# Kernel optimization log

Measured on AMD Instinct MI355X. Metric: run time of the kernel, lower is better.

The kernel has to match this reference:

```python
import jax, jax.numpy as jnp
import numpy as np

B, XD, ZD, XE, H, NH = 8192, 4096, 1024, 64, 128, 4
NUM_STEPS, STEP, NOISE = 10, 0.01, 1.0
EPS = 1e-5


def setup_inputs() -> dict:
    key = jax.random.key(0)
    ks = jax.random.split(key, 16)
    w = lambda k, s: jax.random.normal(k, s, jnp.float32) * 0.02
    inp = {"x": jax.random.normal(ks[0], (B, XD), jnp.float32)}
    inp.update(
        px_W1=w(ks[1], (H, ZD)), px_b1=jnp.zeros(H, jnp.float32),
        px_W2=w(ks[2], (XD, H)), px_b2=jnp.zeros(XD, jnp.float32),
        emb_W=w(ks[3], (XE, XD)), emb_b=jnp.zeros(XE, jnp.float32),
        xp_W=w(ks[4], (H, XE)), xp_b=jnp.zeros(H, jnp.float32),
        zp_W=w(ks[5], (H, ZD)), zp_b=jnp.zeros(H, jnp.float32),
        sa_Wqkv=w(ks[6], (3 * H, H)), sa_bqkv=jnp.zeros(3 * H, jnp.float32),
        sa_Wo=w(ks[7], (H, H)), sa_bo=jnp.zeros(H, jnp.float32),
        ca_Wqkv=w(ks[8], (3 * H, H)), ca_bqkv=jnp.zeros(3 * H, jnp.float32),
        ca_Wo=w(ks[9], (H, H)), ca_bo=jnp.zeros(H, jnp.float32),
        ffn_W1=w(ks[10], (H, H)), ffn_b1=jnp.zeros(H, jnp.float32),
        ffn_W2=w(ks[11], (H, H)), ffn_b2=jnp.zeros(H, jnp.float32),
        ln1_g=jnp.ones(H, jnp.float32), ln1_b=jnp.zeros(H, jnp.float32),
        ln2_g=jnp.ones(H, jnp.float32), ln2_b=jnp.zeros(H, jnp.float32),
        ln3_g=jnp.ones(H, jnp.float32), ln3_b=jnp.zeros(H, jnp.float32),
        out_W=w(ks[12], (1, H)), out_b=jnp.zeros(1, jnp.float32),
    )
    return inp


def _ln(x, g, b):
    m = jnp.mean(x, -1, keepdims=True)
    v = jnp.var(x, -1, keepdims=True)
    return (x - m) * jax.lax.rsqrt(v + EPS) * g + b


def _mha(q, k, v, Wqkv, bqkv, Wo, bo):
    # torch nn.MultiheadAttention math, batch-first layout (B, S, E)
    E = q.shape[-1]
    d = E // NH
    Wq, Wk, Wv = jnp.split(Wqkv, 3, 0)
    bq, bk, bv = jnp.split(bqkv, 3, 0)
    hd = lambda t, W, bb: (t @ W.T + bb).reshape(t.shape[0], t.shape[1], NH, d)
    qh, kh, vh = hd(q, Wq, bq), hd(k, Wk, bk), hd(v, Wv, bv)
    s = jnp.einsum('bqhd,bkhd->bhqk', qh, kh) / jnp.sqrt(jnp.float32(d))
    a = jax.nn.softmax(s, -1)
    o = jnp.einsum('bhqk,bkhd->bqhd', a, vh).reshape(q.shape[0], q.shape[1], E)
    return o @ Wo.T + bo


def _forward(x, px_W1, px_b1, px_W2, px_b2, emb_W, emb_b, xp_W, xp_b, zp_W, zp_b,
             sa_Wqkv, sa_bqkv, sa_Wo, sa_bo, ca_Wqkv, ca_bqkv, ca_Wo, ca_bo,
             ffn_W1, ffn_b1, ffn_W2, ffn_b2, ln1_g, ln1_b, ln2_g, ln2_b,
             ln3_g, ln3_b, out_W, out_b):
    bsz = x.shape[0]
    px = lambda z: jax.nn.relu(z @ px_W1.T + px_b1) @ px_W2.T + px_b2
    grad_fn = jax.grad(lambda z: jnp.sum((px(z) - x) ** 2))
    ks = jax.random.split(jax.random.key(42), NUM_STEPS + 1)
    z0 = jax.random.normal(ks[0], (bsz, ZD), jnp.float32)

    def step(z, k):
        z = z - 0.5 * STEP * grad_fn(z)
        z = z + NOISE * jnp.sqrt(jnp.float32(STEP)) * jax.random.normal(k, z.shape, z.dtype)
        return z, None

    z, _ = jax.lax.scan(step, z0, ks[1:])
    z = jax.lax.stop_gradient(z)  # torch: z.detach()

    x_recon = px(z)                               # (B, XD)
    x_tok = (x @ emb_W.T + emb_b)[:, None, :]     # (B, 1, XE)
    z_lat = z[:, None, :]                         # (B, 1, ZD)
    x_h = x_tok @ xp_W.T + xp_b                   # (B, 1, H)
    z_h = z_lat @ zp_W.T + zp_b                   # (B, 1, H)
    sa = _mha(x_h, x_h, x_h, sa_Wqkv, sa_bqkv, sa_Wo, sa_bo)
    h1 = _ln(x_h + sa, ln1_g, ln1_b)
    ca = _mha(h1, z_h, z_h, ca_Wqkv, ca_bqkv, ca_Wo, ca_bo)
    h2 = _ln(h1 + ca, ln2_g, ln2_b)
    ff = jax.nn.relu(h2 @ ffn_W1.T + ffn_b1) @ ffn_W2.T + ffn_b2
    h3 = _ln(h2 + ff, ln3_g, ln3_b)
    y_pred = h3 @ out_W.T + out_b                 # (B, 1, 1)
    return x_recon, y_pred


def reference(x, px_W1, px_b1, px_W2, px_b2, emb_W, emb_b, xp_W, xp_b, zp_W, zp_b,
              sa_Wqkv, sa_bqkv, sa_Wo, sa_bo, ca_Wqkv, ca_bqkv, ca_Wo, ca_bo,
              ffn_W1, ffn_b1, ffn_W2, ffn_b2, ln1_g, ln1_b, ln2_g, ln2_b,
              ln3_g, ln3_b, out_W, out_b):
    return _forward(x, px_W1, px_b1, px_W2, px_b2, emb_W, emb_b, xp_W, xp_b,
                    zp_W, zp_b, sa_Wqkv, sa_bqkv, sa_Wo, sa_bo, ca_Wqkv,
                    ca_bqkv, ca_Wo, ca_bo, ffn_W1, ffn_b1, ffn_W2, ffn_b2,
                    ln1_g, ln1_b, ln2_g, ln2_b, ln3_g, ln3_b, out_W, out_b)
```

## Files before the change

### kernel.cpp

```cpp
#include <hip/hip_runtime.h>
#include <hip/hip_bf16.h>
#include <cstdint>
#include <cstddef>
#include <cmath>

#define B_     8192
#define XD_    4096
#define ZD_    1024
#define XE_    64
#define H_     128
#define ZN_    (B_*ZD_)

typedef __attribute__((ext_vector_type(8))) short short8_t;
typedef __attribute__((ext_vector_type(4))) float f32x4_t;
#define MFMA16(a,b,c) __builtin_amdgcn_mfma_f32_16x16x32_bf16((a),(b),(c),0,0,0)

__host__ __device__ __forceinline__ uint32_t rotl32_(uint32_t x, int r){ return (x<<r)|(x>>(32-r)); }

__host__ __device__ __forceinline__ void tf2x32(uint32_t k0, uint32_t k1,
                                                uint32_t x0, uint32_t x1,
                                                uint32_t* o0, uint32_t* o1){
  uint32_t k2 = k0 ^ k1 ^ 0x1BD11BDAu;
  x0 += k0; x1 += k1;
  x0 += x1; x1 = rotl32_(x1,13); x1 ^= x0;
  x0 += x1; x1 = rotl32_(x1,15); x1 ^= x0;
  x0 += x1; x1 = rotl32_(x1,26); x1 ^= x0;
  x0 += x1; x1 = rotl32_(x1, 6); x1 ^= x0;
  x0 += k1; x1 += k2 + 1u;
  x0 += x1; x1 = rotl32_(x1,17); x1 ^= x0;
  x0 += x1; x1 = rotl32_(x1,29); x1 ^= x0;
  x0 += x1; x1 = rotl32_(x1,16); x1 ^= x0;
  x0 += x1; x1 = rotl32_(x1,24); x1 ^= x0;
  x0 += k2; x1 += k0 + 2u;
  x0 += x1; x1 = rotl32_(x1,13); x1 ^= x0;
  x0 += x1; x1 = rotl32_(x1,15); x1 ^= x0;
  x0 += x1; x1 = rotl32_(x1,26); x1 ^= x0;
  x0 += x1; x1 = rotl32_(x1, 6); x1 ^= x0;
  x0 += k0; x1 += k1 + 3u;
  x0 += x1; x1 = rotl32_(x1,17); x1 ^= x0;
  x0 += x1; x1 = rotl32_(x1,29); x1 ^= x0;
  x0 += x1; x1 = rotl32_(x1,16); x1 ^= x0;
  x0 += x1; x1 = rotl32_(x1,24); x1 ^= x0;
  x0 += k1; x1 += k2 + 4u;
  x0 += x1; x1 = rotl32_(x1,13); x1 ^= x0;
  x0 += x1; x1 = rotl32_(x1,15); x1 ^= x0;
  x0 += x1; x1 = rotl32_(x1,26); x1 ^= x0;
  x0 += x1; x1 = rotl32_(x1, 6); x1 ^= x0;
  x0 += k2; x1 += k0 + 5u;
  *o0 = x0; *o1 = x1;
}

__device__ __forceinline__ float erfinv_(float x){
  float w = -__logf(fmaf(-x, x, 1.0f));
  float p;
  if (w < 5.0f){
    w -= 2.5f;
    p = 2.81022636e-08f;
    p = fmaf(p, w, 3.43273939e-07f);
    p = fmaf(p, w, -3.5233877e-06f);
    p = fmaf(p, w, -4.39150654e-06f);
    p = fmaf(p, w, 0.00021858087f);
    p = fmaf(p, w, -0.00125372503f);
    p = fmaf(p, w, -0.00417768164f);
    p = fmaf(p, w, 0.246640727f);
    p = fmaf(p, w, 1.50140941f);
  } else {
    w = sqrtf(w) - 3.0f;
    p = -0.000200214257f;
    p = fmaf(p, w, 0.000100950558f);
    p = fmaf(p, w, 0.00134934322f);
    p = fmaf(p, w, -0.00367342844f);
    p = fmaf(p, w, 0.00573950773f);
    p = fmaf(p, w, -0.0076224613f);
    p = fmaf(p, w, 0.00943887047f);
    p = fmaf(p, w, 1.00167406f);
    p = fmaf(p, w, 2.83297682f);
  }
  return p * x;
}

__device__ __forceinline__ float bits_to_normal(uint32_t bits){
  float f = __uint_as_float((bits >> 9) | 0x3f800000u) - 1.0f;
  float u = fmaxf(-0.99999994f, fmaf(f, 2.0f, -0.99999994f));
  return 1.41421356f * erfinv_(u);
}

__device__ __forceinline__ float rng_normal(uint32_t k0, uint32_t k1, uint32_t idx){
  uint32_t o0, o1; tf2x32(k0, k1, 0u, idx, &o0, &o1);
  return bits_to_normal(o0 ^ o1);
}

__device__ __forceinline__ ushort f2bf(float f){
  return __builtin_bit_cast(ushort, __float2bfloat16(f));
}

__global__ void k_prepA(const float* __restrict__ saWo, const float* __restrict__ saWqkv,
                        const float* __restrict__ caWo, const float* __restrict__ caWqkv,
                        float* __restrict__ S, float* __restrict__ U){
  int blk = blockIdx.x, tid = threadIdx.x;
  int idx = (blk & 255) * 64 + tid;
  int i = idx >> 7, j = idx & 127;
  if (blk < 256){
    float acc = (i == j) ? 1.0f : 0.0f;
    for (int k = 0; k < H_; ++k) acc += saWo[i*H_ + k] * saWqkv[(2*H_ + k)*H_ + j];
    S[idx] = acc;
  } else {
    float acc = 0.0f;
    for (int k = 0; k < H_; ++k) acc += caWo[i*H_ + k] * caWqkv[(2*H_ + k)*H_ + j];
    U[idx] = acc;
  }
}

__global__ void k_prepB(const float* __restrict__ saWo, const float* __restrict__ sabqkv, const float* __restrict__ sabo,
                        const float* __restrict__ caWo, const float* __restrict__ cabqkv, const float* __restrict__ cabo,
                        const float* __restrict__ W2, const float* __restrict__ pb2,
                        float* __restrict__ s0, float* __restrict__ u0, float* __restrict__ cb,
                        uint32_t* __restrict__ dkeys){
  int blk = blockIdx.x, tid = threadIdx.x;
  if (blk == 0 && tid == 0){
    for (uint32_t i = 0; i < 11; ++i){
      uint32_t a, b; tf2x32(0u, 42u, 0u, i, &a, &b);
      dkeys[2*i] = a; dkeys[2*i+1] = b;
    }
  }
  if (blk < 2){
    int i = blk*64 + tid;
    float acc = sabo[i];
    for (int k = 0; k < H_; ++k) acc += saWo[i*H_ + k] * sabqkv[2*H_ + k];
    s0[i] = acc;
  } else if (blk < 4){
    int i = (blk-2)*64 + tid;
    float acc = cabo[i];
    for (int k = 0; k < H_; ++k) acc += caWo[i*H_ + k] * cabqkv[2*H_ + k];
    u0[i] = acc;
  } else {
    int j = (blk-4)*64 + tid;
    float acc = 0.0f;
    for (int c = 0; c < XD_; ++c) acc += pb2[c] * W2[(size_t)c*H_ + j];
    cb[j] = acc;
  }
}

__global__ void k_prepM(const float* __restrict__ W2, float* __restrict__ M){
  int idx = blockIdx.x*64 + threadIdx.x;
  int j1 = idx >> 7, j2 = idx & 127;
  float acc = 0.0f;
  for (int c = 0; c < XD_; ++c) acc += W2[(size_t)c*H_ + j1] * W2[(size_t)c*H_ + j2];
  M[idx] = acc;
}

__global__ void k_prepTR(const float* __restrict__ S, const float* __restrict__ U,
                         const float* __restrict__ xpW, const float* __restrict__ zpW,
                         const float* __restrict__ xpb, const float* __restrict__ zpb,
                         const float* __restrict__ s0, const float* __restrict__ u0,
                         float* __restrict__ T, float* __restrict__ R,
                         float* __restrict__ t0, float* __restrict__ r0v){
  int blk = blockIdx.x, tid = threadIdx.x;
  if (blk < 128){
    int idx = blk*64 + tid;
    int i = idx >> 6, e = idx & 63;
    float acc = 0.0f;
    for (int m = 0; m < H_; ++m) acc += S[i*H_ + m] * xpW[m*XE_ + e];
    T[idx] = acc;
  } else if (blk < 2176){
    int idx = (blk-128)*64 + tid;
    int i = idx >> 10, k = idx & 1023;
    float acc = 0.0f;
    for (int m = 0; m < H_; ++m) acc += U[i*H_ + m] * zpW[(size_t)m*ZD_ + k];
    R[idx] = acc;
  } else if (blk < 2178){
    int i = (blk-2176)*64 + tid;
    float acc = s0[i];
    for (int m = 0; m < H_; ++m) acc += S[i*H_ + m] * xpb[m];
    t0[i] = acc;
  } else {
    int i = (blk-2178)*64 + tid;
    float acc = u0[i];
    for (int m = 0; m < H_; ++m) acc += U[i*H_ + m] * zpb[m];
    r0v[i] = acc;
  }
}

__global__ void k_prepWXT(const float* __restrict__ W2, const float* __restrict__ T,
                          const float* __restrict__ embW, const float* __restrict__ embb,
                          const float* __restrict__ t0,
                          ushort* __restrict__ WXT, float* __restrict__ q0){
  int idx = blockIdx.x*256 + threadIdx.x;
  int j = idx >> 12, c = idx & 4095;
  float v;
  if (j < H_) v = W2[(size_t)c*H_ + j];
  else {
    int i = j - H_;
    float acc = 0.0f;
    for (int e = 0; e < XE_; ++e) acc += T[i*XE_ + e] * embW[(size_t)e*XD_ + c];
    v = acc;
  }
  WXT[idx] = f2bf(v);
  if (idx < H_){
    float acc = t0[idx];
    for (int e = 0; e < XE_; ++e) acc += T[idx*XE_ + e] * embb[e];
    q0[idx] = acc;
  }
}

__global__ void k_conv(const float* __restrict__ W2, const float* __restrict__ W1,
                       const float* __restrict__ Mm, const float* __restrict__ R,
                       ushort* __restrict__ W2bf, ushort* __restrict__ W1bf,
                       ushort* __restrict__ W1Tbf, ushort* __restrict__ Mbf,
                       ushort* __restrict__ FBT){
  int idx = blockIdx.x*256 + threadIdx.x;
  if (idx < 524288) W2bf[idx] = f2bf(W2[idx]);
  else if (idx < 655360){ int i = idx - 524288; W1bf[i] = f2bf(W1[i]); }
  else if (idx < 786432){ int i = idx - 655360; int k = i >> 7, h = i & 127;
    W1Tbf[i] = f2bf(W1[h*ZD_ + k]); }
  else if (idx < 802816){ int i = idx - 786432; Mbf[i] = f2bf(Mm[i]); }
  else { int i = idx - 802816; int j = i >> 10, k = i & 1023;
    FBT[i] = f2bf(j < H_ ? W1[j*ZD_ + k] : R[(size_t)(j-H_)*ZD_ + k]); }
}

__global__ __launch_bounds__(256) void k_xpass_mfma(
    const float* __restrict__ x, const ushort* __restrict__ WXT,
    const float* __restrict__ cb, const float* __restrict__ q0,
    float* __restrict__ cneg, float* __restrict__ h1pre){
  __shared__ __align__(16) ushort xt[2][32*72];
  __shared__ __align__(16) ushort bt[2][128*72];
  const int t = threadIdx.x, lane = t & 63, w = t >> 6;
  const int bm = blockIdx.x >> 1, bn = blockIdx.x & 1;
  const int row0 = bm*32, ncol0 = bn*128;
  const int l15 = lane & 15, kq8 = (lane >> 4)*8, rq = (lane >> 4)*4;
  const int rt = w & 1, cb4 = (w >> 1)*4;
  const int xr = t >> 3, xk = (t & 7)*8;
  const int wn = t >> 1, wk = (t & 1)*32;
  f32x4_t acc[4] = {};
  {
    float4 v0 = *(const float4*)&x[(size_t)(row0+xr)*XD_ + xk];
    float4 v1 = *(const float4*)&x[(size_t)(row0+xr)*XD_ + xk + 4];
    union { ushort u[8]; uint4 q; } p;
    p.u[0]=f2bf(v0.x); p.u[1]=f2bf(v0.y); p.u[2]=f2bf(v0.z); p.u[3]=f2bf(v0.w);
    p.u[4]=f2bf(v1.x); p.u[5]=f2bf(v1.y); p.u[6]=f2bf(v1.z); p.u[7]=f2bf(v1.w);
    *(uint4*)&xt[0][xr*72 + xk] = p.q;
    const ushort* s = &WXT[(size_t)(ncol0+wn)*XD_ + wk];
    uint4 b0v=*(const uint4*)s, b1v=*(const uint4*)(s+8), b2v=*(const uint4*)(s+16), b3v=*(const uint4*)(s+24);
    ushort* d = &bt[0][wn*72 + wk];
    *(uint4*)d=b0v; *(uint4*)(d+8)=b1v; *(uint4*)(d+16)=b2v; *(uint4*)(d+24)=b3v;
  }
  float4 xv0, xv1; uint4 wb0, wb1, wb2, wb3;
  {
    xv0 = *(const float4*)&x[(size_t)(row0+xr)*XD_ + 64 + xk];
    xv1 = *(const float4*)&x[(size_t)(row0+xr)*XD_ + 64 + xk + 4];
    const ushort* s = &WXT[(size_t)(ncol0+wn)*XD_ + 64 + wk];
    wb0=*(const uint4*)s; wb1=*(const uint4*)(s+8); wb2=*(const uint4*)(s+16); wb3=*(const uint4*)(s+24);
  }
  #pragma unroll 1
  for (int it = 0; it < 64; ++it){
    __syncthreads();
    if (it < 63){
      union { ushort u[8]; uint4 q; } p;
      p.u[0]=f2bf(xv0.x); p.u[1]=f2bf(xv0.y); p.u[2]=f2bf(xv0.z); p.u[3]=f2bf(xv0.w);
      p.u[4]=f2bf(xv1.x); p.u[5]=f2bf(xv1.y); p.u[6]=f2bf(xv1.z); p.u[7]=f2bf(xv1.w);
      *(uint4*)&xt[(it+1)&1][xr*72 + xk] = p.q;
      ushort* d = &bt[(it+1)&1][wn*72 + wk];
      *(uint4*)d=wb0; *(uint4*)(d+8)=wb1; *(uint4*)(d+16)=wb2; *(uint4*)(d+24)=wb3;
    }
    if (it < 62){
      const int kt = (it+2)*64;
      xv0 = *(const float4*)&x[(size_t)(row0+xr)*XD_ + kt + xk];
      xv1 = *(const float4*)&x[(size_t)(row0+xr)*XD_ + kt + xk + 4];
      const ushort* s = &WXT[(size_t)(ncol0+wn)*XD_ + kt + wk];
      wb0=*(const uint4*)s; wb1=*(const uint4*)(s+8); wb2=*(const uint4*)(s+16); wb3=*(const uint4*)(s+24);
    }
    const ushort* xb = &xt[it&1][(rt*16+l15)*72];
    const ushort* bb = &bt[it&1][0];
    #pragma unroll
    for (int h = 0; h < 2; ++h){
      short8_t a = *(const short8_t*)(xb + h*32 + kq8);
      #pragma unroll
      for (int c = 0; c < 4; ++c){
        short8_t b = *(const short8_t*)(bb + ((cb4+c)*16+l15)*72 + h*32 + kq8);
        acc[c] = MFMA16(a, b, acc[c]);
      }
    }
  }
  #pragma unroll
  for (int c = 0; c < 4; ++c){
    int jl = (cb4+c)*16 + l15;
    #pragma unroll
    for (int r = 0; r < 4; ++r){
      int row = row0 + rt*16 + rq + r;
      float v = acc[c][r];
      if (bn == 0) cneg[(size_t)row*H_ + jl] = 2.0f*(cb[jl] - v);
      else         h1pre[(size_t)row*H_ + jl] = v + q0[jl];
    }
  }
}

__global__ __launch_bounds__(512) void k_langevin(
    const ushort* __restrict__ W1bf, const ushort* __restrict__ W1Tbf,
    const ushort* __restrict__ Mbf, const ushort* __restrict__ FBT,
    const float* __restrict__ b1, const float* __restrict__ r0v,
    const float* __restrict__ cneg, const uint32_t* __restrict__ dkeys,
    ushort* __restrict__ hfin_bf, float* __restrict__ capre){
  __shared__ __align__(16) float  zlds[16][1028];
  __shared__ __align__(16) ushort zbf[16][1032];
  __shared__ __align__(16) ushort ws_[2][128*72];
  __shared__ __align__(16) ushort abuf[16*136];
  __shared__ __align__(16) ushort glbuf[16*136];

  const int t = threadIdx.x, lane = t & 63, w = t >> 6;
  const int l15 = lane & 15, kq8 = (lane >> 4)*8, rq = (lane >> 4)*4;
  const int b0 = blockIdx.x * 16;
  const int myc = w*16 + l15;

  {
    const uint32_t k0 = dkeys[0], k1 = dkeys[1];
    const int row16 = t >> 5, c4 = (t & 31)*4;
    #pragma unroll 1
    for (int i = 0; i < 8; ++i){
      const int col = c4 + 128*i;
      uint32_t base = (uint32_t)(b0 + row16)*1024u + (uint32_t)col;
      float4 v;
      v.x = rng_normal(k0,k1,base+0);
      v.y = rng_normal(k0,k1,base+1);
      v.z = rng_normal(k0,k1,base+2);
      v.w = rng_normal(k0,k1,base+3);
      *(float4*)&zlds[row16][col] = v;
      ushort4 b4; b4.x=f2bf(v.x); b4.y=f2bf(v.y); b4.z=f2bf(v.z); b4.w=f2bf(v.w);
      *(ushort4*)&zbf[row16][col] = b4;
    }
  }
  const float bb = b1[myc];
  float cn[4];
  #pragma unroll
  for (int r = 0; r < 4; ++r) cn[r] = cneg[(size_t)(b0+rq+r)*H_ + myc];

  const int wr = t >> 2, wk4 = (t & 3)*16;
  const int kk3 = (t & 3)*32;

  #pragma unroll 1
  for (int s = 0; s < 10; ++s){
    const uint32_t nk0 = dkeys[2+2*s], nk1 = dkeys[3+2*s];
    {
      const ushort* sw = &W1bf[(size_t)wr*ZD_ + wk4];
      uint4 a0 = *(const uint4*)sw, a1 = *(const uint4*)(sw+8);
      ushort* d = &ws_[0][wr*72 + wk4];
      *(uint4*)d = a0; *(uint4*)(d+8) = a1;
    }
    uint4 p0, p1;
    {
      const ushort* sw = &W1bf[(size_t)wr*ZD_ + 64 + wk4];
      p0 = *(const uint4*)sw; p1 = *(const uint4*)(sw+8);
    }
    f32x4_t acc = {};
    #pragma unroll 1
    for (int it = 0; it < 16; ++it){
      __syncthreads();
      if (it < 15){
        ushort* d = &ws_[(it+1)&1][wr*72 + wk4];
        *(uint4*)d = p0; *(uint4*)(d+8) = p1;
      }
      if (it < 14){
        const ushort* sw = &W1bf[(size_t)wr*ZD_ + (it+2)*64 + wk4];
        p0 = *(const uint4*)sw; p1 = *(const uint4*)(sw+8);
      }
      const ushort* wsb = &ws_[it&1][myc*72];
      #pragma unroll
      for (int h = 0; h < 2; ++h){
        short8_t av = *(const short8_t*)&zbf[l15][it*64 + h*32 + kq8];
        short8_t bv = *(const short8_t*)(wsb + h*32 + kq8);
        acc = MFMA16(av, bv, acc);
      }
    }
    float hv[4];
    #pragma unroll
    for (int r = 0; r < 4; ++r){
      hv[r] = acc[r] + bb;
      abuf[(rq+r)*136 + myc] = f2bf(hv[r] > 0.f ? hv[r] : 0.f);
    }
    __syncthreads();
    {
      const ushort* sm = &Mbf[(size_t)wr*H_ + kk3];
      uint4 m0=*(const uint4*)sm, m1=*(const uint4*)(sm+8), m2=*(const uint4*)(sm+16), m3=*(const uint4*)(sm+24);
      ushort* d = &ws_[kk3>>6][wr*72 + (kk3&63)];
      *(uint4*)d=m0; *(uint4*)(d+8)=m1; *(uint4*)(d+16)=m2; *(uint4*)(d+24)=m3;
    }
    __syncthreads();
    f32x4_t acc2 = {};
    #pragma unroll
    for (int c = 0; c < 2; ++c)
      #pragma unroll
      for (int h = 0; h < 2; ++h){
        short8_t av = *(const short8_t*)&abuf[l15*136 + c*64 + h*32 + kq8];
        short8_t bv = *(const short8_t*)&ws_[c][myc*72 + h*32 + kq8];
        acc2 = MFMA16(av, bv, acc2);
      }
    #pragma unroll
    for (int r = 0; r < 4; ++r){
      float g = (hv[r] > 0.f) ? fmaf(2.f, acc2[r], cn[r]) : 0.f;
      glbuf[(rq+r)*136 + myc] = f2bf(g);
    }
    uint4 v0, v1, v2, v3;
    {
      const ushort* sw = &W1Tbf[(size_t)wr*H_ + kk3];
      v0=*(const uint4*)sw; v1=*(const uint4*)(sw+8); v2=*(const uint4*)(sw+16); v3=*(const uint4*)(sw+24);
    }
    #pragma unroll 1
    for (int nt = 0; nt < 8; ++nt){
      __syncthreads();
      {
        ushort* d = &ws_[kk3>>6][wr*72 + (kk3&63)];
        *(uint4*)d=v0; *(uint4*)(d+8)=v1; *(uint4*)(d+16)=v2; *(uint4*)(d+24)=v3;
      }
      if (nt < 7){
        const ushort* sw = &W1Tbf[(size_t)((nt+1)*128 + wr)*H_ + kk3];
        v0=*(const uint4*)sw; v1=*(const uint4*)(sw+8); v2=*(const uint4*)(sw+16); v3=*(const uint4*)(sw+24);
      }
      __syncthreads();
      f32x4_t acc3 = {};
      #pragma unroll
      for (int c = 0; c < 2; ++c)
        #pragma unroll
        for (int h = 0; h < 2; ++h){
          short8_t av = *(const short8_t*)&glbuf[l15*136 + c*64 + h*32 + kq8];
          short8_t bv = *(const short8_t*)&ws_[c][myc*72 + h*32 + kq8];
          acc3 = MFMA16(av, bv, acc3);
        }
      const int col = nt*128 + myc;
      #pragma unroll
      for (int r = 0; r < 4; ++r){
        const int row = rq + r;
        uint32_t idx = (uint32_t)(b0+row)*1024u + (uint32_t)col;
        float t2 = fmaf(-0.005f, acc3[r], zlds[row][col]);
        float zn = fmaf(0.1f, rng_normal(nk0,nk1,idx), t2);
        zlds[row][col] = zn;
        zbf[row][col] = f2bf(zn);
      }
    }
    __syncthreads();
  }

  f32x4_t fac0 = {}, fac1 = {};
  const int n2 = t >> 1, kh = (t & 1)*32;
  uint4 c0, c1, c2, c3;
  {
    const ushort* sf = &FBT[(size_t)n2*ZD_ + kh];
    c0=*(const uint4*)sf; c1=*(const uint4*)(sf+8); c2=*(const uint4*)(sf+16); c3=*(const uint4*)(sf+24);
  }
  #pragma unroll 1
  for (int it = 0; it < 16; ++it){
    __syncthreads();
    {
      ushort* d = (n2 < 128) ? &ws_[0][n2*72 + kh] : &ws_[1][(n2-128)*72 + kh];
      *(uint4*)d=c0; *(uint4*)(d+8)=c1; *(uint4*)(d+16)=c2; *(uint4*)(d+24)=c3;
    }
    if (it < 15){
      const ushort* sf = &FBT[(size_t)n2*ZD_ + (it+1)*64 + kh];
      c0=*(const uint4*)sf; c1=*(const uint4*)(sf+8); c2=*(const uint4*)(sf+16); c3=*(const uint4*)(sf+24);
    }
    __syncthreads();
    #pragma unroll
    for (int h = 0; h < 2; ++h){
      short8_t av = *(const short8_t*)&zbf[l15][it*64 + h*32 + kq8];
      short8_t bv0 = *(const short8_t*)&ws_[0][myc*72 + h*32 + kq8];
      fac0 = MFMA16(av, bv0, fac0);
      short8_t bv1 = *(const short8_t*)&ws_[1][myc*72 + h*32 + kq8];
      fac1 = MFMA16(av, bv1, fac1);
    }
  }
  {
    const float rv = r0v[myc];
    #pragma unroll
    for (int r = 0; r < 4; ++r){
      int row = b0 + rq + r;
      float h0 = fac0[r] + bb;
      hfin_bf[(size_t)row*H_ + myc] = f2bf(h0 > 0.f ? h0 : 0.f);
      capre[(size_t)row*H_ + myc] = fac1[r] + rv;
    }
  }
}

__global__ __launch_bounds__(256) void k_xrecon_mfma(
    const ushort* __restrict__ hfin_bf, const ushort* __restrict__ W2bf,
    const float* __restrict__ b2, float* __restrict__ out){
  __shared__ __align__(16) ushort at[64*136];
  __shared__ __align__(16) ushort bt[128*136];
  const int tid = threadIdx.x, lane = tid & 63, w = tid >> 6;
  const int bm = blockIdx.x >> 5, bn = blockIdx.x & 31;
  const int row0 = bm*64, c0 = bn*128;
  const int l15 = lane & 15, kq8 = (lane >> 4)*8, rq = (lane >> 4)*4;
  { int r = tid >> 2, kq = (tid & 3)*32;
    const ushort* src = &hfin_bf[(size_t)(row0 + r)*H_ + kq];
    #pragma unroll
    for (int i = 0; i < 4; ++i) *(uint4*)&at[r*136 + kq + 8*i] = *(const uint4*)(src + 8*i);
  }
  { int n = tid >> 1, kh = (tid & 1)*64;
    const ushort* src = &W2bf[(size_t)(c0 + n)*H_ + kh];
    #pragma unroll
    for (int i = 0; i < 8; ++i) *(uint4*)&bt[n*136 + kh + 8*i] = *(const uint4*)(src + 8*i);
  }
  __syncthreads();
  f32x4_t acc[8] = {};
  #pragma unroll
  for (int k = 0; k < 4; ++k){
    short8_t a = *(const short8_t*)&at[(w*16 + l15)*136 + k*32 + kq8];
    #pragma unroll
    for (int nf = 0; nf < 8; ++nf){
      short8_t b = *(const short8_t*)&bt[(nf*16 + l15)*136 + k*32 + kq8];
      acc[nf] = MFMA16(a, b, acc[nf]);
    }
  }
  #pragma unroll
  for (int nf = 0; nf < 8; ++nf){
    int c = c0 + nf*16 + l15;
    float bbv = b2[c];
    #pragma unroll
    for (int r = 0; r < 4; ++r){
      int row = row0 + w*16 + rq + r;
      out[(size_t)row*XD_ + c] = acc[nf][r] + bbv;
    }
  }
}

__device__ __forceinline__ float wsum64(float v){
  #pragma unroll
  for (int off = 32; off > 0; off >>= 1) v += __shfl_xor(v, off, 64);
  return v;
}

__global__ __launch_bounds__(256) void k_tail(
    const float* __restrict__ h1pre, const float* __restrict__ capre,
    const float* __restrict__ ln1g, const float* __restrict__ ln1b,
    const float* __restrict__ ln2g, const float* __restrict__ ln2b,
    const float* __restrict__ ln3g, const float* __restrict__ ln3b,
    const float* __restrict__ fW1, const float* __restrict__ fb1,
    const float* __restrict__ fW2, const float* __restrict__ fb2,
    const float* __restrict__ outW, const float* __restrict__ outb,
    float* __restrict__ y){
  __shared__ float sh2[4][128];
  __shared__ float st1[4][128];
  const int tid = threadIdx.x;
  const int w = tid >> 6;
  const int l = tid & 63;
  const int b = blockIdx.x * 4 + w;
  const float* hp = h1pre + (size_t)b * H_;
  const float* cp = capre + (size_t)b * H_;
  float x0 = hp[l], x1 = hp[l+64];
  float m = wsum64(x0 + x1) * (1.0f/128.0f);
  float d0 = x0 - m, d1 = x1 - m;
  float v = wsum64(d0*d0 + d1*d1) * (1.0f/128.0f);
  float rs = rsqrtf(v + 1e-5f);
  float h1a = d0 * rs * ln1g[l]    + ln1b[l];
  float h1b = d1 * rs * ln1g[l+64] + ln1b[l+64];
  x0 = h1a + cp[l]; x1 = h1b + cp[l+64];
  m = wsum64(x0 + x1) * (1.0f/128.0f);
  d0 = x0 - m; d1 = x1 - m;
  v = wsum64(d0*d0 + d1*d1) * (1.0f/128.0f);
  rs = rsqrtf(v + 1e-5f);
  float h2a = d0 * rs * ln2g[l]    + ln2b[l];
  float h2b = d1 * rs * ln2g[l+64] + ln2b[l+64];
  sh2[w][l] = h2a; sh2[w][l+64] = h2b;
  __syncthreads();
  float ta = fb1[l], tb = fb1[l+64];
  #pragma unroll 8
  for (int m4 = 0; m4 < H_; m4 += 4){
    float4 hv = *(const float4*)&sh2[w][m4];
    float4 wa = *(const float4*)&fW1[(size_t)l*H_ + m4];
    float4 wb = *(const float4*)&fW1[(size_t)(l+64)*H_ + m4];
    ta = fmaf(wa.x, hv.x, ta); ta = fmaf(wa.y, hv.y, ta); ta = fmaf(wa.z, hv.z, ta); ta = fmaf(wa.w, hv.w, ta);
    tb = fmaf(wb.x, hv.x, tb); tb = fmaf(wb.y, hv.y, tb); tb = fmaf(wb.z, hv.z, tb); tb = fmaf(wb.w, hv.w, tb);
  }
  ta = fmaxf(ta, 0.0f); tb = fmaxf(tb, 0.0f);
  st1[w][l] = ta; st1[w][l+64] = tb;
  __syncthreads();
  float fa = fb2[l], fbv = fb2[l+64];
  #pragma unroll 8
  for (int m4 = 0; m4 < H_; m4 += 4){
    float4 tv = *(const float4*)&st1[w][m4];
    float4 wa = *(const float4*)&fW2[(size_t)l*H_ + m4];
    float4 wb = *(const float4*)&fW2[(size_t)(l+64)*H_ + m4];
    fa  = fmaf(wa.x, tv.x, fa);  fa  = fmaf(wa.y, tv.y, fa);  fa  = fmaf(wa.z, tv.z, fa);  fa  = fmaf(wa.w, tv.w, fa);
    fbv = fmaf(wb.x, tv.x, fbv); fbv = fmaf(wb.y, tv.y, fbv); fbv = fmaf(wb.z, tv.z, fbv); fbv = fmaf(wb.w, tv.w, fbv);
  }
  x0 = h2a + fa; x1 = h2b + fbv;
  m = wsum64(x0 + x1) * (1.0f/128.0f);
  d0 = x0 - m; d1 = x1 - m;
  v = wsum64(d0*d0 + d1*d1) * (1.0f/128.0f);
  rs = rsqrtf(v + 1e-5f);
  float h3a = d0 * rs * ln3g[l]    + ln3b[l];
  float h3b = d1 * rs * ln3g[l+64] + ln3b[l+64];
  float py = wsum64(outW[l]*h3a + outW[l+64]*h3b);
  if (l == 0) y[b] = py + outb[0];
}

extern "C" void kernel_launch(void* const* d_in, const int* in_sizes, int n_in,
                              void* d_out, int out_size, void* d_ws, size_t ws_size,
                              hipStream_t stream){
  const float* x      = (const float*)d_in[0];
  const float* pxW1   = (const float*)d_in[1];
  const float* pxb1   = (const float*)d_in[2];
  const float* pxW2   = (const float*)d_in[3];
  const float* pxb2   = (const float*)d_in[4];
  const float* embW   = (const float*)d_in[5];
  const float* embb   = (const float*)d_in[6];
  const float* xpW    = (const float*)d_in[7];
  const float* xpb    = (const float*)d_in[8];
  const float* zpW    = (const float*)d_in[9];
  const float* zpb    = (const float*)d_in[10];
  const float* saWqkv = (const float*)d_in[11];
  const float* sabqkv = (const float*)d_in[12];
  const float* saWo   = (const float*)d_in[13];
  const float* sabo   = (const float*)d_in[14];
  const float* caWqkv = (const float*)d_in[15];
  const float* cabqkv = (const float*)d_in[16];
  const float* caWo   = (const float*)d_in[17];
  const float* cabo   = (const float*)d_in[18];
  const float* fW1    = (const float*)d_in[19];
  const float* fb1    = (const float*)d_in[20];
  const float* fW2    = (const float*)d_in[21];
  const float* fb2    = (const float*)d_in[22];
  const float* ln1g   = (const float*)d_in[23];
  const float* ln1b   = (const float*)d_in[24];
  const float* ln2g   = (const float*)d_in[25];
  const float* ln2b   = (const float*)d_in[26];
  const float* ln3g   = (const float*)d_in[27];
  const float* ln3b   = (const float*)d_in[28];
  const float* outW   = (const float*)d_in[29];
  const float* outb   = (const float*)d_in[30];
  (void)in_sizes; (void)n_in; (void)out_size; (void)ws_size;

  float* ws    = (float*)d_ws;
  float* cneg  = ws;
  float* h1pre = cneg + (size_t)B_*H_;
  float* capre = h1pre + (size_t)B_*H_;
  float* Rm    = capre + (size_t)B_*H_;
  float* Mm    = Rm + (size_t)H_*ZD_;
  float* Sm    = Mm + H_*H_;
  float* Um    = Sm + H_*H_;
  float* Tm    = Um + H_*H_;
  float* vs0   = Tm + H_*XE_;
  float* vu0   = vs0 + H_;
  float* vt0   = vu0 + H_;
  float* vq0   = vt0 + H_;
  float* vr0   = vq0 + H_;
  float* vcb   = vr0 + H_;
  uint32_t* dkeys = (uint32_t*)(vcb + H_);
  ushort* WXT   = (ushort*)(dkeys + 32);
  ushort* W2bf  = WXT + (size_t)256*XD_;
  ushort* W1bf  = W2bf + (size_t)XD_*H_;
  ushort* W1Tbf = W1bf + (size_t)H_*ZD_;
  ushort* Mbf   = W1Tbf + (size_t)ZD_*H_;
  ushort* FBT   = Mbf + H_*H_;
  ushort* hfin  = FBT + (size_t)256*ZD_;

  float* xre   = (float*)d_out;
  float* ypred = xre + (size_t)B_*XD_;

  k_prepA   <<<512,  64, 0, stream>>>(saWo, saWqkv, caWo, caWqkv, Sm, Um);
  k_prepB   <<<6,    64, 0, stream>>>(saWo, sabqkv, sabo, caWo, cabqkv, cabo, pxW2, pxb2,
                                      vs0, vu0, vcb, dkeys);
  k_prepM   <<<256,  64, 0, stream>>>(pxW2, Mm);
  k_prepTR  <<<2180, 64, 0, stream>>>(Sm, Um, xpW, zpW, xpb, zpb, vs0, vu0, Tm, Rm, vt0, vr0);
  k_prepWXT <<<4096, 256, 0, stream>>>(pxW2, Tm, embW, embb, vt0, WXT, vq0);
  k_conv    <<<4160, 256, 0, stream>>>(pxW2, pxW1, Mm, Rm, W2bf, W1bf, W1Tbf, Mbf, FBT);
  k_xpass_mfma <<<512, 256, 0, stream>>>(x, WXT, vcb, vq0, cneg, h1pre);
  k_langevin <<<512, 512, 0, stream>>>(W1bf, W1Tbf, Mbf, FBT, pxb1, vr0, cneg, dkeys, hfin, capre);
  k_xrecon_mfma <<<4096, 256, 0, stream>>>(hfin, W2bf, pxb2, xre);
  k_tail    <<<2048, 256, 0, stream>>>(h1pre, capre, ln1g, ln1b, ln2g, ln2b, ln3g, ln3b,
                                       fW1, fb1, fW2, fb2, outW, outb, ypred);
}
```

Before: 919.8 us.

## Run Langevin dynamics in projected 256-dim space using precomputed Gram matrices

```diff
diff --git a/kernel.cpp b/kernel.cpp
--- a/kernel.cpp
+++ b/kernel.cpp
@@ -93,6 +93,7 @@
 __device__ __forceinline__ ushort f2bf(float f){
   return __builtin_bit_cast(ushort, __float2bfloat16(f));
 }
+__device__ __forceinline__ float bf2f(ushort u){ return __uint_as_float(((uint32_t)u) << 16); }
 
 __global__ void k_prepA(const float* __restrict__ saWo, const float* __restrict__ saWqkv,
                         const float* __restrict__ caWo, const float* __restrict__ caWqkv,
@@ -205,17 +206,26 @@
 
 __global__ void k_conv(const float* __restrict__ W2, const float* __restrict__ W1,
                        const float* __restrict__ Mm, const float* __restrict__ R,
-                       ushort* __restrict__ W2bf, ushort* __restrict__ W1bf,
-                       ushort* __restrict__ W1Tbf, ushort* __restrict__ Mbf,
+                       ushort* __restrict__ W2bf, ushort* __restrict__ Mbf,
                        ushort* __restrict__ FBT){
   int idx = blockIdx.x*256 + threadIdx.x;
   if (idx < 524288) W2bf[idx] = f2bf(W2[idx]);
-  else if (idx < 655360){ int i = idx - 524288; W1bf[i] = f2bf(W1[i]); }
-  else if (idx < 786432){ int i = idx - 655360; int k = i >> 7, h = i & 127;
-    W1Tbf[i] = f2bf(W1[h*ZD_ + k]); }
-  else if (idx < 802816){ int i = idx - 786432; Mbf[i] = f2bf(Mm[i]); }
-  else { int i = idx - 802816; int j = i >> 10, k = i & 1023;
+  else if (idx < 540672){ int i = idx - 524288; Mbf[i] = f2bf(2.0f*Mm[i]); }
+  else { int i = idx - 540672; int j = i >> 10, k = i & 1023;
     FBT[i] = f2bf(j < H_ ? W1[j*ZD_ + k] : R[(size_t)(j-H_)*ZD_ + k]); }
+}
+
+__global__ void k_prepG(const float* __restrict__ W1, const float* __restrict__ R,
+                        ushort* __restrict__ GGr){
+  int idx = blockIdx.x*64 + threadIdx.x;
+  int i = idx >> 7, k = idx & 127;
+  float acc = 0.0f;
+  if (i < 128){
+    for (int m = 0; m < ZD_; ++m) acc += W1[(size_t)i*ZD_ + m] * W1[(size_t)k*ZD_ + m];
+  } else {
+    for (int m = 0; m < ZD_; ++m) acc += W1[(size_t)k*ZD_ + m] * R[(size_t)(i-128)*ZD_ + m];
+  }
+  GGr[idx] = f2bf(-0.005f * acc);
 }
 
 __global__ __launch_bounds__(256) void k_xpass_mfma(
@@ -294,187 +304,144 @@
   }
 }
 
-__global__ __launch_bounds__(512) void k_langevin(
-    const ushort* __restrict__ W1bf, const ushort* __restrict__ W1Tbf,
-    const ushort* __restrict__ Mbf, const ushort* __restrict__ FBT,
+__global__ __launch_bounds__(256) void k_noiseproj(
+    const ushort* __restrict__ FBT, const uint32_t* __restrict__ dkeys,
+    float* __restrict__ y0c0, ushort* __restrict__ NWR){
+  __shared__ __align__(16) ushort at[64*72];
+  const int t = threadIdx.x, lane = t & 63, w = t >> 6;
+  const int l15 = lane & 15, kq8 = (lane >> 4)*8, rq = (lane >> 4)*4;
+  const int p = blockIdx.x >> 7, mb = blockIdx.x & 127;
+  const int gb0 = mb*64;
+  const uint32_t k0 = dkeys[2*p], k1 = dkeys[2*p+1];
+  const int arow = t >> 2, ak0 = (t & 3)*16;
+  f32x4_t acc[16] = {};
+  #pragma unroll 1
+  for (int it = 0; it < 16; ++it){
+    __syncthreads();
+    {
+      uint32_t base = (uint32_t)(gb0 + arow)*1024u + (uint32_t)(it*64 + ak0);
+      union { ushort u[8]; uint4 q; } pk;
+      #pragma unroll
+      for (int j = 0; j < 8; ++j) pk.u[j] = f2bf(rng_normal(k0,k1,base+j));
+      *(uint4*)&at[arow*72 + ak0] = pk.q;
+      #pragma unroll
+      for (int j = 0; j < 8; ++j) pk.u[j] = f2bf(rng_normal(k0,k1,base+8+j));
+      *(uint4*)&at[arow*72 + ak0 + 8] = pk.q;
+    }
+    __syncthreads();
+    #pragma unroll
+    for (int h = 0; h < 2; ++h){
+      short8_t a = *(const short8_t*)&at[(w*16+l15)*72 + h*32 + kq8];
+      #pragma unroll
+      for (int cf = 0; cf < 16; ++cf){
+        short8_t b = *(const short8_t*)&FBT[(size_t)(cf*16+l15)*ZD_ + it*64 + h*32 + kq8];
+        acc[cf] = MFMA16(a, b, acc[cf]);
+      }
+    }
+  }
+  #pragma unroll
+  for (int cf = 0; cf < 16; ++cf){
+    int col = cf*16 + l15;
+    #pragma unroll
+    for (int r = 0; r < 4; ++r){
+      int row = gb0 + w*16 + rq + r;
+      float v = acc[cf][r];
+      if (p == 0) y0c0[(size_t)row*256 + col] = v;
+      else NWR[(size_t)(p-1)*2097152 + (size_t)row*256 + col] = f2bf(0.1f*v);
+    }
+  }
+}
+
+__global__ __launch_bounds__(512) void k_lv2(
+    const ushort* __restrict__ M2bf, const ushort* __restrict__ GGr,
+    const float* __restrict__ y0c0, const ushort* __restrict__ NWR,
     const float* __restrict__ b1, const float* __restrict__ r0v,
-    const float* __restrict__ cneg, const uint32_t* __restrict__ dkeys,
+    const float* __restrict__ cneg,
     ushort* __restrict__ hfin_bf, float* __restrict__ capre){
-  __shared__ __align__(16) float  zlds[16][1028];
-  __shared__ __align__(16) ushort zbf[16][1032];
-  __shared__ __align__(16) ushort ws_[2][128*72];
   __shared__ __align__(16) ushort abuf[16*136];
   __shared__ __align__(16) ushort glbuf[16*136];
-
   const int t = threadIdx.x, lane = t & 63, w = t >> 6;
   const int l15 = lane & 15, kq8 = (lane >> 4)*8, rq = (lane >> 4)*4;
   const int b0 = blockIdx.x * 16;
   const int myc = w*16 + l15;
-
-  {
-    const uint32_t k0 = dkeys[0], k1 = dkeys[1];
-    const int row16 = t >> 5, c4 = (t & 31)*4;
-    #pragma unroll 1
-    for (int i = 0; i < 8; ++i){
-      const int col = c4 + 128*i;
-      uint32_t base = (uint32_t)(b0 + row16)*1024u + (uint32_t)col;
-      float4 v;
-      v.x = rng_normal(k0,k1,base+0);
-      v.y = rng_normal(k0,k1,base+1);
-      v.z = rng_normal(k0,k1,base+2);
-      v.w = rng_normal(k0,k1,base+3);
-      *(float4*)&zlds[row16][col] = v;
-      ushort4 b4; b4.x=f2bf(v.x); b4.y=f2bf(v.y); b4.z=f2bf(v.z); b4.w=f2bf(v.w);
-      *(ushort4*)&zbf[row16][col] = b4;
-    }
-  }
-  const float bb = b1[myc];
+  const int col2 = w*32 + l15;
+
+  f32x4_t acc[2];
+  #pragma unroll
+  for (int nf = 0; nf < 2; ++nf)
+    #pragma unroll
+    for (int r = 0; r < 4; ++r)
+      acc[nf][r] = y0c0[(size_t)(b0+rq+r)*256 + col2 + nf*16];
   float cn[4];
   #pragma unroll
   for (int r = 0; r < 4; ++r) cn[r] = cneg[(size_t)(b0+rq+r)*H_ + myc];
-
-  const int wr = t >> 2, wk4 = (t & 3)*16;
-  const int kk3 = (t & 3)*32;
+  float bb2[2];
+  bb2[0] = (w < 4) ? b1[col2] : 0.0f;
+  bb2[1] = (w < 4) ? b1[col2+16] : 0.0f;
+  ushort nx[8];
+  #pragma unroll
+  for (int nf = 0; nf < 2; ++nf)
+    #pragma unroll
+    for (int r = 0; r < 4; ++r)
+      nx[nf*4+r] = NWR[(size_t)(b0+rq+r)*256 + col2 + nf*16];
 
   #pragma unroll 1
   for (int s = 0; s < 10; ++s){
-    const uint32_t nk0 = dkeys[2+2*s], nk1 = dkeys[3+2*s];
-    {
-      const ushort* sw = &W1bf[(size_t)wr*ZD_ + wk4];
-      uint4 a0 = *(const uint4*)sw, a1 = *(const uint4*)(sw+8);
-      ushort* d = &ws_[0][wr*72 + wk4];
-      *(uint4*)d = a0; *(uint4*)(d+8) = a1;
-    }
-    uint4 p0, p1;
-    {
-      const ushort* sw = &W1bf[(size_t)wr*ZD_ + 64 + wk4];
-      p0 = *(const uint4*)sw; p1 = *(const uint4*)(sw+8);
-    }
-    f32x4_t acc = {};
-    #pragma unroll 1
-    for (int it = 0; it < 16; ++it){
-      __syncthreads();
-      if (it < 15){
-        ushort* d = &ws_[(it+1)&1][wr*72 + wk4];
-        *(uint4*)d = p0; *(uint4*)(d+8) = p1;
+    if (w < 4){
+      #pragma unroll
+      for (int nf = 0; nf < 2; ++nf)
+        #pragma unroll
+        for (int r = 0; r < 4; ++r)
+          abuf[(rq+r)*136 + col2 + nf*16] = f2bf(fmaxf(acc[nf][r] + bb2[nf], 0.0f));
+    }
+    __syncthreads();
+    f32x4_t g2 = {};
+    #pragma unroll
+    for (int h = 0; h < 4; ++h){
+      short8_t a = *(const short8_t*)&abuf[l15*136 + h*32 + kq8];
+      short8_t b = *(const short8_t*)&M2bf[(size_t)myc*H_ + h*32 + kq8];
+      g2 = MFMA16(a, b, g2);
+    }
+    #pragma unroll
+    for (int r = 0; r < 4; ++r){
+      float g = (abuf[(rq+r)*136 + myc] != 0) ? (g2[r] + cn[r]) : 0.0f;
+      glbuf[(rq+r)*136 + myc] = f2bf(g);
+    }
+    __syncthreads();
+    #pragma unroll
+    for (int nf = 0; nf < 2; ++nf)
+      #pragma unroll
+      for (int h = 0; h < 4; ++h){
+        short8_t a = *(const short8_t*)&glbuf[l15*136 + h*32 + kq8];
+        short8_t b = *(const short8_t*)&GGr[(size_t)(col2 + nf*16)*H_ + h*32 + kq8];
+        acc[nf] = MFMA16(a, b, acc[nf]);
       }
-      if (it < 14){
-        const ushort* sw = &W1bf[(size_t)wr*ZD_ + (it+2)*64 + wk4];
-        p0 = *(const uint4*)sw; p1 = *(const uint4*)(sw+8);
-      }
-      const ushort* wsb = &ws_[it&1][myc*72];
-      #pragma unroll
-      for (int h = 0; h < 2; ++h){
-        short8_t av = *(const short8_t*)&zbf[l15][it*64 + h*32 + kq8];
-        short8_t bv = *(const short8_t*)(wsb + h*32 + kq8);
-        acc = MFMA16(av, bv, acc);
-      }
-    }
-    float hv[4];
-    #pragma unroll
-    for (int r = 0; r < 4; ++r){
-      hv[r] = acc[r] + bb;
-      abuf[(rq+r)*136 + myc] = f2bf(hv[r] > 0.f ? hv[r] : 0.f);
+    #pragma unroll
+    for (int nf = 0; nf < 2; ++nf)
+      #pragma unroll
+      for (int r = 0; r < 4; ++r)
+        acc[nf][r] += bf2f(nx[nf*4+r]);
+    if (s < 9){
+      #pragma unroll
+      for (int nf = 0; nf < 2; ++nf)
+        #pragma unroll
+        for (int r = 0; r < 4; ++r)
+          nx[nf*4+r] = NWR[(size_t)(s+1)*2097152 + (size_t)(b0+rq+r)*256 + col2 + nf*16];
     }
     __syncthreads();
-    {
-      const ushort* sm = &Mbf[(size_t)wr*H_ + kk3];
-      uint4 m0=*(const uint4*)sm, m1=*(const uint4*)(sm+8), m2=*(const uint4*)(sm+16), m3=*(const uint4*)(sm+24);
-      ushort* d = &ws_[kk3>>6][wr*72 + (kk3&63)];
-      *(uint4*)d=m0; *(uint4*)(d+8)=m1; *(uint4*)(d+16)=m2; *(uint4*)(d+24)=m3;
-    }
-    __syncthreads();
-    f32x4_t acc2 = {};
-    #pragma unroll
-    for (int c = 0; c < 2; ++c)
-      #pragma unroll
-      for (int h = 0; h < 2; ++h){
-        short8_t av = *(const short8_t*)&abuf[l15*136 + c*64 + h*32 + kq8];
-        short8_t bv = *(const short8_t*)&ws_[c][myc*72 + h*32 + kq8];
-        acc2 = MFMA16(av, bv, acc2);
-      }
-    #pragma unroll
-    for (int r = 0; r < 4; ++r){
-      float g = (hv[r] > 0.f) ? fmaf(2.f, acc2[r], cn[r]) : 0.f;
-      glbuf[(rq+r)*136 + myc] = f2bf(g);
-    }
-    uint4 v0, v1, v2, v3;
-    {
-      const ushort* sw = &W1Tbf[(size_t)wr*H_ + kk3];
-      v0=*(const uint4*)sw; v1=*(const uint4*)(sw+8); v2=*(const uint4*)(sw+16); v3=*(const uint4*)(sw+24);
-    }
-    #pragma unroll 1
-    for (int nt = 0; nt < 8; ++nt){
-      __syncthreads();
-      {
-        ushort* d = &ws_[kk3>>6][wr*72 + (kk3&63)];
-        *(uint4*)d=v0; *(uint4*)(d+8)=v1; *(uint4*)(d+16)=v2; *(uint4*)(d+24)=v3;
-      }
-      if (nt < 7){
-        const ushort* sw = &W1Tbf[(size_t)((nt+1)*128 + wr)*H_ + kk3];
-        v0=*(const uint4*)sw; v1=*(const uint4*)(sw+8); v2=*(const uint4*)(sw+16); v3=*(const uint4*)(sw+24);
-      }
-      __syncthreads();
-      f32x4_t acc3 = {};
-      #pragma unroll
-      for (int c = 0; c < 2; ++c)
-        #pragma unroll
-        for (int h = 0; h < 2; ++h){
-          short8_t av = *(const short8_t*)&glbuf[l15*136 + c*64 + h*32 + kq8];
-          short8_t bv = *(const short8_t*)&ws_[c][myc*72 + h*32 + kq8];
-          acc3 = MFMA16(av, bv, acc3);
-        }
-      const int col = nt*128 + myc;
-      #pragma unroll
-      for (int r = 0; r < 4; ++r){
-        const int row = rq + r;
-        uint32_t idx = (uint32_t)(b0+row)*1024u + (uint32_t)col;
-        float t2 = fmaf(-0.005f, acc3[r], zlds[row][col]);
-        float zn = fmaf(0.1f, rng_normal(nk0,nk1,idx), t2);
-        zlds[row][col] = zn;
-        zbf[row][col] = f2bf(zn);
-      }
-    }
-    __syncthreads();
-  }
-
-  f32x4_t fac0 = {}, fac1 = {};
-  const int n2 = t >> 1, kh = (t & 1)*32;
-  uint4 c0, c1, c2, c3;
-  {
-    const ushort* sf = &FBT[(size_t)n2*ZD_ + kh];
-    c0=*(const uint4*)sf; c1=*(const uint4*)(sf+8); c2=*(const uint4*)(sf+16); c3=*(const uint4*)(sf+24);
-  }
-  #pragma unroll 1
-  for (int it = 0; it < 16; ++it){
-    __syncthreads();
-    {
-      ushort* d = (n2 < 128) ? &ws_[0][n2*72 + kh] : &ws_[1][(n2-128)*72 + kh];
-      *(uint4*)d=c0; *(uint4*)(d+8)=c1; *(uint4*)(d+16)=c2; *(uint4*)(d+24)=c3;
-    }
-    if (it < 15){
-      const ushort* sf = &FBT[(size_t)n2*ZD_ + (it+1)*64 + kh];
-      c0=*(const uint4*)sf; c1=*(const uint4*)(sf+8); c2=*(const uint4*)(sf+16); c3=*(const uint4*)(sf+24);
-    }
-    __syncthreads();
-    #pragma unroll
-    for (int h = 0; h < 2; ++h){
-      short8_t av = *(const short8_t*)&zbf[l15][it*64 + h*32 + kq8];
-      short8_t bv0 = *(const short8_t*)&ws_[0][myc*72 + h*32 + kq8];
-      fac0 = MFMA16(av, bv0, fac0);
-      short8_t bv1 = *(const short8_t*)&ws_[1][myc*72 + h*32 + kq8];
-      fac1 = MFMA16(av, bv1, fac1);
-    }
-  }
-  {
-    const float rv = r0v[myc];
-    #pragma unroll
-    for (int r = 0; r < 4; ++r){
-      int row = b0 + rq + r;
-      float h0 = fac0[r] + bb;
-      hfin_bf[(size_t)row*H_ + myc] = f2bf(h0 > 0.f ? h0 : 0.f);
-      capre[(size_t)row*H_ + myc] = fac1[r] + rv;
-    }
+  }
+  if (w < 4){
+    #pragma unroll
+    for (int nf = 0; nf < 2; ++nf)
+      #pragma unroll
+      for (int r = 0; r < 4; ++r)
+        hfin_bf[(size_t)(b0+rq+r)*H_ + col2 + nf*16] = f2bf(fmaxf(acc[nf][r] + bb2[nf], 0.0f));
+  } else {
+    #pragma unroll
+    for (int nf = 0; nf < 2; ++nf)
+      #pragma unroll
+      for (int r = 0; r < 4; ++r)
+        capre[(size_t)(b0+rq+r)*H_ + (col2 + nf*16 - 128)] = acc[nf][r] + r0v[col2 + nf*16 - 128];
   }
 }
 
@@ -643,13 +610,14 @@
   float* vr0   = vq0 + H_;
   float* vcb   = vr0 + H_;
   uint32_t* dkeys = (uint32_t*)(vcb + H_);
-  ushort* WXT   = (ushort*)(dkeys + 32);
+  float* y0c0  = (float*)(dkeys + 32);
+  ushort* WXT   = (ushort*)(y0c0 + (size_t)B_*256);
   ushort* W2bf  = WXT + (size_t)256*XD_;
-  ushort* W1bf  = W2bf + (size_t)XD_*H_;
-  ushort* W1Tbf = W1bf + (size_t)H_*ZD_;
-  ushort* Mbf   = W1Tbf + (size_t)ZD_*H_;
+  ushort* Mbf   = W2bf + (size_t)XD_*H_;
   ushort* FBT   = Mbf + H_*H_;
-  ushort* hfin  = FBT + (size_t)256*ZD_;
+  ushort* GGr   = FBT + (size_t)256*ZD_;
+  ushort* hfin  = GGr + (size_t)256*H_;
+  ushort* NWR   = hfin + (size_t)B_*H_;
 
   float* xre   = (float*)d_out;
   float* ypred = xre + (size_t)B_*XD_;
@@ -660,9 +628,11 @@
   k_prepM   <<<256,  64, 0, stream>>>(pxW2, Mm);
   k_prepTR  <<<2180, 64, 0, stream>>>(Sm, Um, xpW, zpW, xpb, zpb, vs0, vu0, Tm, Rm, vt0, vr0);
   k_prepWXT <<<4096, 256, 0, stream>>>(pxW2, Tm, embW, embb, vt0, WXT, vq0);
-  k_conv    <<<4160, 256, 0, stream>>>(pxW2, pxW1, Mm, Rm, W2bf, W1bf, W1Tbf, Mbf, FBT);
+  k_conv    <<<3136, 256, 0, stream>>>(pxW2, pxW1, Mm, Rm, W2bf, Mbf, FBT);
+  k_prepG   <<<512,  64, 0, stream>>>(pxW1, Rm, GGr);
+  k_noiseproj <<<1408, 256, 0, stream>>>(FBT, dkeys, y0c0, NWR);
   k_xpass_mfma <<<512, 256, 0, stream>>>(x, WXT, vcb, vq0, cneg, h1pre);
-  k_langevin <<<512, 512, 0, stream>>>(W1bf, W1Tbf, Mbf, FBT, pxb1, vr0, cneg, dkeys, hfin, capre);
+  k_lv2     <<<512, 512, 0, stream>>>(Mbf, GGr, y0c0, NWR, pxb1, vr0, cneg, hfin, capre);
   k_xrecon_mfma <<<4096, 256, 0, stream>>>(hfin, W2bf, pxb2, xre);
   k_tail    <<<2048, 256, 0, stream>>>(h1pre, capre, ln1g, ln1b, ln2g, ln2b, ln3g, ln3b,
                                        fW1, fb1, fW2, fb2, outW, outb, ypred);
```

Result: faster. 900.2 us (-2.1%).
